# Performance work log

Measured on AMD Instinct MI355X. Metric: run time of the kernel, lower is better.

## Reference

```python
import jax, jax.numpy as jnp
import numpy as np

N, E, G = 8000, 128000, 4
C, NLM, NL = 64, 16, 4
NEL, NB, NH = 10, 8, 64
RMAX = 5.0
PCUT = 5.0
AVG_NEIGH = 16.0
SIGMA = 1.0
LBOX = 6.0
KR = 3
T = 2
LMAP = jnp.array([0, 1, 1, 1, 2, 2, 2, 2, 2, 3, 3, 3, 3, 3, 3, 3])


def _nvec():
    r = np.arange(-KR, KR + 1)
    n = np.stack(np.meshgrid(r, r, r, indexing='ij'), -1).reshape(-1, 3)
    n = n[np.any(n != 0, axis=1)]  # [342,3], k=0 excluded
    return jnp.asarray(n, jnp.float32)


def sph_harm(u):
    # component-normalized real spherical harmonics up to l=3, unit input u [E,3]
    x, y, z = u[:, 0], u[:, 1], u[:, 2]
    one = jnp.ones_like(x)
    c3, c5, c15 = 3.0 ** 0.5, 5.0 ** 0.5, 15.0 ** 0.5
    Y = [one,
         c3 * x, c3 * y, c3 * z,
         c15 * x * y, c15 * y * z, 0.5 * c5 * (3 * z * z - 1.0), c15 * x * z, 0.5 * c15 * (x * x - y * y),
         (35.0 / 8.0) ** 0.5 * y * (3 * x * x - y * y), 105.0 ** 0.5 * x * y * z,
         (21.0 / 8.0) ** 0.5 * y * (5 * z * z - 1.0), 0.5 * 7.0 ** 0.5 * z * (5 * z * z - 3.0),
         (21.0 / 8.0) ** 0.5 * x * (5 * z * z - 1.0), 0.5 * 105.0 ** 0.5 * z * (x * x - y * y),
         (35.0 / 8.0) ** 0.5 * x * (x * x - 3 * y * y)]
    return jnp.stack(Y, -1)  # [E,16]


def radial_basis(r):
    # Bessel basis * polynomial cutoff (MACE RadialEmbeddingBlock)
    u = r / RMAX
    n = jnp.arange(1, NB + 1, dtype=jnp.float32)
    bes = (2.0 / RMAX) ** 0.5 * jnp.sin(n[None, :] * jnp.pi * u[:, None]) / (r[:, None] + 1e-9)
    p = PCUT
    fc = 1.0 - 0.5 * (p + 1) * (p + 2) * u ** p + p * (p + 2) * u ** (p + 1) - 0.5 * p * (p + 1) * u ** (p + 2)
    fc = fc * (u < 1.0)
    return bes * fc[:, None]  # [E,8]


def setup_inputs() -> dict:
    key = jax.random.key(0)
    ks = jax.random.split(key, 24)

    def p(k, shape, fan_in):
        return jax.random.normal(k, shape, jnp.float32) / (fan_in ** 0.5)

    elem = jax.random.randint(ks[0], (N,), 0, NEL)
    inp = {
        'node_attrs': jax.nn.one_hot(elem, NEL, dtype=jnp.float32),
        'positions': jax.random.uniform(ks[1], (N, 3), jnp.float32) * LBOX,
        'shifts': jnp.zeros((E, 3), jnp.float32),
        'density_coefficients': jax.random.normal(ks[2], (N, 1), jnp.float32) * 0.1,
        'cell': jnp.tile(jnp.eye(3, dtype=jnp.float32) * LBOX, (G, 1, 1)),
        'rcell': jnp.tile(jnp.eye(3, dtype=jnp.float32) / LBOX, (G, 1, 1)),
        'volume': jnp.full((G,), LBOX ** 3, jnp.float32),
        'edge_index': jax.random.randint(ks[3], (2, E), 0, N),
        'batch': jnp.repeat(jnp.arange(G), N // G),
        'emb_W': p(ks[4], (NEL, C), NEL),
        'q_coef': p(ks[5], (T, C), 1),
        'rad_W1': p(ks[6], (T, NB, NH), NB),
        'rad_W2': p(ks[7], (T, NH, NH), NH),
        'rad_W3': p(ks[8], (T, NH, NH), NH),
        'rad_W4': p(ks[9], (T, NH, C * NL), NH),
        'lin_up': p(ks[10], (T, NL, C, C), C),
        'lin_out': p(ks[11], (T, NL, C, C), C),
        'W_sc': p(ks[12], (T, NEL, C, C), C),
        'Wp': p(ks[13], (T, 3, C, C), C),
        'W_read0': p(ks[14], (C,), C),
        'Wread1_a': p(ks[15], (C, 16), C),
        'Wread1_b': p(ks[16], (16,), 16),
        'Wq_read': p(ks[17], (T, C), C),
        'atomic_E': jax.random.normal(ks[18], (NEL,), jnp.float32),
    }
    return inp


def reference(node_attrs, positions, shifts, density_coefficients, cell, rcell, volume,
              edge_index, batch, emb_W, q_coef, rad_W1, rad_W2, rad_W3, rad_W4,
              lin_up, lin_out, W_sc, Wp, W_read0, Wread1_a, Wread1_b, Wq_read, atomic_E):
    sender, receiver = edge_index[0], edge_index[1]
    vec = positions[receiver] - positions[sender] + shifts
    r = jnp.linalg.norm(vec, axis=-1)
    Y = sph_harm(vec / (r[:, None] + 1e-9))      # [E,16]
    ef = radial_basis(r)                          # [E,8]

    q = density_coefficients                      # [N,1], max_l=0 multipoles
    feats = jnp.zeros((N, C, NLM), jnp.float32).at[:, :, 0].set(node_attrs @ emb_W)
    e0 = jax.ops.segment_sum(node_attrs @ atomic_E, batch, G)
    energies = [e0]

    for t in range(T):
        # charge-coefficient injection (charge_coefs_linears)
        feats = feats.at[:, :, 0].add(q * q_coef[t][None, :])
        # per-l linear up
        h = jnp.einsum('ncl,lcd->ndl', feats, lin_up[t][LMAP])
        # radial MLP -> per-edge, per-channel, per-l tensor-product weights
        w = jax.nn.silu(ef @ rad_W1[t])
        w = jax.nn.silu(w @ rad_W2[t])
        w = jax.nn.silu(w @ rad_W3[t])
        w = (w @ rad_W4[t]).reshape(E, C, NL)[:, :, LMAP]   # [E,C,16]
        # depthwise equivariant TP message: gather -> contract -> modulate
        hj = h[sender]                                       # [E,C,16]
        s_e = jnp.einsum('ecl,el->ec', hj, Y)                # edge invariant
        m = w * (Y[:, None, :] * s_e[:, :, None])            # [E,C,16]
        A = jax.ops.segment_sum(m, receiver, N) / AVG_NEIGH  # scatter-reduce
        A = jnp.einsum('ncl,lcd->ndl', A, lin_out[t][LMAP])
        # element-dependent residual (self-connection)
        wn = jnp.einsum('nk,kcd->ncd', node_attrs, W_sc[t])
        sc = jnp.einsum('ncd,ncl->ndl', wn, feats)
        # product block: correlation-3 symmetric-contraction surrogate
        s1 = jnp.sum(A * A, axis=2)                           # [N,C]
        out = (jnp.einsum('ncl,cd->ndl', A, Wp[t, 0])
               + jnp.einsum('ncl,cd->ndl', A * s1[:, :, None], Wp[t, 1])
               + jnp.einsum('ncl,cd->ndl', A * (s1 * s1)[:, :, None], Wp[t, 2]))
        feats = out + sc
        # readout
        if t == T - 1:
            node_e = jax.nn.silu(feats[:, :, 0] @ Wread1_a) @ Wread1_b
        else:
            node_e = feats[:, :, 0] @ W_read0
        node_e = node_e + q[:, 0] * (feats[:, :, 0] @ Wq_read[t])
        energies.append(jax.ops.segment_sum(node_e, batch, G))

    # k-space (Ewald-like) electrostatics with Gaussian-smeared charges
    nv = _nvec()                                              # [K,3]
    kvec = 2.0 * jnp.pi * jnp.einsum('kj,gji->gki', nv, rcell)  # [G,K,3]
    k2 = jnp.sum(kvec * kvec, -1)                             # [G,K]
    phase = jnp.einsum('ni,nki->nk', positions, kvec[batch])  # [N,K]
    Sr = jax.ops.segment_sum(q * jnp.cos(phase), batch, G)
    Si = jax.ops.segment_sum(q * jnp.sin(phase), batch, G)
    filt = jnp.exp(-0.5 * SIGMA * SIGMA * k2) / k2
    Ees = (2.0 * jnp.pi / volume) * jnp.sum(filt * (Sr * Sr + Si * Si), axis=1)

    total_energy = jnp.sum(jnp.stack(energies, -1), -1) + Ees
    total_charge = jax.ops.segment_sum(q[:, 0], batch, G)
    dipole = jax.ops.segment_sum(q * positions, batch, G)
    return total_energy, total_charge, dipole
```

## Files before the change

kernel.cpp:

```cpp
#include <hip/hip_runtime.h>
#include <hip/hip_bf16.h>

constexpr int N    = 8000;
constexpr int E    = 128000;
constexpr int G    = 4;
constexpr int NEL  = 10;
constexpr int NGR  = N / G;
constexpr int NC   = N * 64;
constexpr int NK   = 342;
constexpr float RMAX = 5.0f;
constexpr int HS = 72;
constexpr int WS2 = 260;
constexpr int WT_T = 25088;

typedef __bf16 bf16x8 __attribute__((ext_vector_type(8)));
typedef float  f32x4v __attribute__((ext_vector_type(4)));
typedef unsigned short u16x8 __attribute__((ext_vector_type(8)));

__device__ __forceinline__ int lmap_rt(int l) { return (l >= 1) + (l >= 4) + (l >= 9); }
__device__ __forceinline__ float silu(float x) { return x / (1.f + __expf(-x)); }
__device__ __forceinline__ float bf2f(unsigned short u) { return __uint_as_float(((unsigned)u) << 16); }
__device__ __forceinline__ unsigned short f2bf(float f) {
    __hip_bfloat16 h = __float2bfloat16(f);
    return *(unsigned short*)&h;
}

__device__ __forceinline__ void mfma_stage(const unsigned short* hsrc, const unsigned short* wt,
                                           int m0, int lane, f32x4v acc[4], bool k8only)
{
    const int quad = lane >> 4;
    const int idx  = lane & 15;
    bf16x8 bz;
    #pragma unroll
    for (int i = 0; i < 8; ++i) bz[i] = (__bf16)0.f;
    bf16x8 a0 = bz, a1 = bz;
    const int mrow = m0 + idx;
    if (k8only) {
        if (quad == 0) a0 = *(const bf16x8*)&hsrc[mrow * HS];
    } else {
        a0 = *(const bf16x8*)&hsrc[mrow * HS + (quad << 3)];
        a1 = *(const bf16x8*)&hsrc[mrow * HS + 32 + (quad << 3)];
    }
    #pragma unroll
    for (int c4 = 0; c4 < 4; ++c4) {
        const int nrow = (c4 << 4) + idx;
        if (k8only) {
            bf16x8 b0 = bz;
            if (quad == 0) b0 = *(const bf16x8*)&wt[nrow * HS];
            acc[c4] = __builtin_amdgcn_mfma_f32_16x16x32_bf16(a0, b0, acc[c4], 0, 0, 0);
        } else {
            const bf16x8 b0 = *(const bf16x8*)&wt[nrow * HS + (quad << 3)];
            const bf16x8 b1 = *(const bf16x8*)&wt[nrow * HS + 32 + (quad << 3)];
            acc[c4] = __builtin_amdgcn_mfma_f32_16x16x32_bf16(a0, b0, acc[c4], 0, 0, 0);
            acc[c4] = __builtin_amdgcn_mfma_f32_16x16x32_bf16(a1, b1, acc[c4], 0, 0, 0);
        }
    }
}

__global__ __launch_bounds__(256) void k_init(const float* __restrict__ na,
    const float* __restrict__ q, const float* __restrict__ pos,
    const int* __restrict__ batch, const float* __restrict__ aE,
    int* __restrict__ elem, int* __restrict__ counts, float* __restrict__ acc)
{
    __shared__ float s[G * 5];
    if (threadIdx.x < G * 5) s[threadIdx.x] = 0.f;
    __syncthreads();
    const int n = blockIdx.x * 256 + threadIdx.x;
    if (n < N) {
        int el = 0; float best = na[n * NEL];
        #pragma unroll
        for (int j = 1; j < NEL; ++j) { float v = na[n * NEL + j]; if (v > best) { best = v; el = j; } }
        elem[n] = el;
        atomicAdd(&counts[el], 1);
        const int g = batch[n];
        const float qn = q[n];
        atomicAdd(&s[g * 5 + 0], aE[el]);
        atomicAdd(&s[g * 5 + 1], qn);
        atomicAdd(&s[g * 5 + 2], qn * pos[n * 3 + 0]);
        atomicAdd(&s[g * 5 + 3], qn * pos[n * 3 + 1]);
        atomicAdd(&s[g * 5 + 4], qn * pos[n * 3 + 2]);
    }
    __syncthreads();
    if (threadIdx.x < G * 5) atomicAdd(&acc[threadIdx.x], s[threadIdx.x]);
}

__global__ __launch_bounds__(256) void k_feat0(const int* __restrict__ elem,
    const float* __restrict__ embW, unsigned short* __restrict__ Fb)
{
    const int i = blockIdx.x * 256 + threadIdx.x;
    if (i < NC) Fb[i] = f2bf(embW[elem[i >> 6] * 64 + (i & 63)]);
}

__global__ void k_offs(const int* __restrict__ counts, int* __restrict__ offs)
{
    if (threadIdx.x == 0 && blockIdx.x == 0) {
        int o = 0;
        for (int j = 0; j < NEL; ++j) { offs[j] = o; o += (counts[j] + 63) & ~63; }
        offs[NEL] = o;
    }
}
__global__ __launch_bounds__(256) void k_scatter(const int* __restrict__ elem,
    const int* __restrict__ offs, int* __restrict__ cursor, int* __restrict__ perm)
{
    const int n = blockIdx.x * 256 + threadIdx.x;
    if (n < N) {
        const int el = elem[n];
        const int p = atomicAdd(&cursor[el], 1);
        perm[offs[el] + p] = n;
    }
}

__global__ __launch_bounds__(256) void k_gcnt(const int* __restrict__ ei, int* __restrict__ cnt)
{
    const int e = blockIdx.x * 256 + threadIdx.x;
    if (e < E) atomicAdd(&cnt[ei[E + e]], 1);
}
__global__ __launch_bounds__(1024) void k_goff(const int* __restrict__ cnt, int* __restrict__ roff)
{
    __shared__ int part[1024];
    const int t = threadIdx.x;
    const int base = t * 8;
    int loc[8];
    int s = 0;
    #pragma unroll
    for (int i = 0; i < 8; ++i) { loc[i] = s; s += (base + i < N) ? cnt[base + i] : 0; }
    part[t] = s;
    __syncthreads();
    for (int d = 1; d < 1024; d <<= 1) {
        const int v = (t >= d) ? part[t - d] : 0;
        __syncthreads();
        part[t] += v;
        __syncthreads();
    }
    const int excl = (t == 0) ? 0 : part[t - 1];
    #pragma unroll
    for (int i = 0; i < 8; ++i) if (base + i < N) roff[base + i] = excl + loc[i];
    if (t == 0) roff[N] = E;
}
__global__ __launch_bounds__(256) void k_gscat(const int* __restrict__ ei,
    const int* __restrict__ roff, int* __restrict__ cur, int* __restrict__ elist)
{
    const int e = blockIdx.x * 256 + threadIdx.x;
    if (e < E) {
        const int rv = ei[E + e];
        const int p = atomicAdd(&cur[rv], 1);
        elist[roff[rv] + p] = e;
    }
}

__global__ __launch_bounds__(256) void k_geom(const float* __restrict__ pos,
    const float* __restrict__ shifts, const int* __restrict__ ei,
    const int* __restrict__ elist, float4* __restrict__ geomv, int* __restrict__ spck)
{
    const int j = blockIdx.x * 256 + threadIdx.x;
    if (j >= E) return;
    const int e = elist[j];
    const int s = ei[e], rv = ei[E + e];
    const float dx = pos[rv * 3 + 0] - pos[s * 3 + 0] + shifts[e * 3 + 0];
    const float dy = pos[rv * 3 + 1] - pos[s * 3 + 1] + shifts[e * 3 + 1];
    const float dz = pos[rv * 3 + 2] - pos[s * 3 + 2] + shifts[e * 3 + 2];
    const float r = sqrtf(dx * dx + dy * dy + dz * dz);
    const float inv = 1.f / (r + 1e-9f);
    float4 g;
    g.x = dx * inv; g.y = dy * inv; g.z = dz * inv; g.w = r;
    geomv[j] = g;
    spck[j] = s;
}

__global__ __launch_bounds__(256) void k_wprep_all(const float* __restrict__ rW1,
    const float* __restrict__ rW2, const float* __restrict__ rW3,
    const float* __restrict__ rW4, const float* __restrict__ Wp,
    const float* __restrict__ lup, const float* __restrict__ lout,
    const float* __restrict__ Wsc,
    unsigned short* __restrict__ WT, unsigned short* __restrict__ WpT,
    unsigned short* __restrict__ WlupT, unsigned short* __restrict__ WloutT,
    unsigned short* __restrict__ WscT)
{
    const int gidx = blockIdx.x * 256 + threadIdx.x;
    if (gidx < 2 * WT_T) {
        const int t = gidx / WT_T;
        const int r = gidx % WT_T;
        float v;
        if (r < 512) {
            const int n = r >> 3, k = r & 7;
            v = rW1[t * 512 + k * 64 + n];
        } else if (r < 4608) {
            const int i = r - 512, n = i >> 6, k = i & 63;
            v = rW2[t * 4096 + k * 64 + n];
        } else if (r < 8704) {
            const int i = r - 4608, n = i >> 6, k = i & 63;
            v = rW3[t * 4096 + k * 64 + n];
        } else {
            const int i = r - 8704, n = i >> 6, k = i & 63;
            v = rW4[t * 16384 + k * 256 + n];
        }
        WT[gidx] = f2bf(v);
    } else if (gidx < 2 * WT_T + 24576) {
        const int idx = gidx - 2 * WT_T;
        const int i  = idx & 4095;
        const int d = i >> 6, c = i & 63;
        WpT[idx] = f2bf(Wp[(size_t)(idx >> 12) * 4096 + c * 64 + d]);
    } else if (gidx < 2 * WT_T + 24576 + 32768) {
        const int idx = gidx - (2 * WT_T + 24576);
        const int i = idx & 4095, d = i >> 6, c = i & 63;
        WlupT[idx] = f2bf(lup[(idx >> 12) * 4096 + c * 64 + d]);
    } else if (gidx < 2 * WT_T + 24576 + 65536) {
        const int idx = gidx - (2 * WT_T + 24576 + 32768);
        const int i = idx & 4095, d = i >> 6, c = i & 63;
        WloutT[idx] = f2bf(lout[(idx >> 12) * 4096 + c * 64 + d]);
    } else if (gidx < 2 * WT_T + 24576 + 65536 + 81920) {
        const int idx = gidx - (2 * WT_T + 24576 + 65536);
        const int i = idx & 4095, d = i >> 6, c = i & 63;
        WscT[idx] = f2bf(Wsc[(idx >> 12) * 4096 + c * 64 + d]);
    }
}

__global__ __launch_bounds__(256) void k_lgemm_hb(unsigned short* __restrict__ Fb,
    const float* __restrict__ q, const float* __restrict__ qc,
    const unsigned short* __restrict__ WT, unsigned short* __restrict__ Hb)
{
    __shared__ unsigned short Xb[64 * HS];
    __shared__ unsigned short Wt[64 * HS];
    const int l  = blockIdx.y;
    const int nb = blockIdx.x << 6;
    const int t  = threadIdx.x;
    const int lane = t & 63;
    const int m0   = (t >> 6) << 4;
    const int quad = lane >> 4;
    const int idx  = lane & 15;
    const int prow = t >> 2, pkb = (t & 3) << 4;
    unsigned short* Xp = Fb + (size_t)l * NC + (size_t)nb * 64;
    if (l == 0) {
        const float qn = q[nb + prow];
        u16x8 x0 = *(const u16x8*)&Xp[prow * 64 + pkb];
        u16x8 x1 = *(const u16x8*)&Xp[prow * 64 + pkb + 8];
        #pragma unroll
        for (int j = 0; j < 8; ++j) {
            x0[j] = f2bf(bf2f(x0[j]) + qn * qc[pkb + j]);
            x1[j] = f2bf(bf2f(x1[j]) + qn * qc[pkb + 8 + j]);
        }
        *(u16x8*)&Xp[prow * 64 + pkb]     = x0;
        *(u16x8*)&Xp[prow * 64 + pkb + 8] = x1;
        *(u16x8*)&Xb[prow * HS + pkb]     = x0;
        *(u16x8*)&Xb[prow * HS + pkb + 8] = x1;
    } else {
        *(u16x8*)&Xb[prow * HS + pkb]     = *(const u16x8*)&Xp[prow * 64 + pkb];
        *(u16x8*)&Xb[prow * HS + pkb + 8] = *(const u16x8*)&Xp[prow * 64 + pkb + 8];
    }
    const unsigned short* W = WT + lmap_rt(l) * 4096;
    *(u16x8*)&Wt[prow * HS + pkb]     = *(const u16x8*)&W[prow * 64 + pkb];
    *(u16x8*)&Wt[prow * HS + pkb + 8] = *(const u16x8*)&W[prow * 64 + pkb + 8];
    __syncthreads();
    f32x4v acc[4];
    #pragma unroll
    for (int c = 0; c < 4; ++c) { acc[c][0] = 0.f; acc[c][1] = 0.f; acc[c][2] = 0.f; acc[c][3] = 0.f; }
    mfma_stage(Xb, Wt, m0, lane, acc, false);
    #pragma unroll
    for (int c4 = 0; c4 < 4; ++c4) {
        #pragma unroll
        for (int r = 0; r < 4; ++r) {
            const int n = nb + m0 + (quad << 2) + r;
            const int col = (c4 << 4) + idx;
            Hb[(size_t)n * 1024 + (l << 6) + col] = f2bf(acc[c4][r]);
        }
    }
}

__global__ __launch_bounds__(256) void k_hbT(const unsigned short* __restrict__ Hb,
    unsigned short* __restrict__ HbT)
{
    const int n = (blockIdx.x << 2) + (threadIdx.x >> 6);
    const int c = threadIdx.x & 63;
    u16x8 a, b;
    #pragma unroll
    for (int l = 0; l < 8; ++l) {
        a[l] = Hb[(size_t)n * 1024 + (l << 6) + c];
        b[l] = Hb[(size_t)n * 1024 + ((l + 8) << 6) + c];
    }
    *(u16x8*)&HbT[(size_t)n * 1024 + c * 16]     = a;
    *(u16x8*)&HbT[(size_t)n * 1024 + c * 16 + 8] = b;
}

__global__ __launch_bounds__(256) void k_lgemm(const float* __restrict__ X,
    const unsigned short* __restrict__ WT, unsigned short* __restrict__ H2b)
{
    __shared__ unsigned short Xb[64 * HS];
    __shared__ unsigned short Wt[64 * HS];
    const int l  = blockIdx.y;
    const int nb = blockIdx.x << 6;
    const int t  = threadIdx.x;
    const int lane = t & 63;
    const int m0   = (t >> 6) << 4;
    const int quad = lane >> 4;
    const int idx  = lane & 15;
    const int prow = t >> 2, pkb = (t & 3) << 4;
    const float* Xp = X + (size_t)l * NC + (size_t)nb * 64;
    #pragma unroll
    for (int k = 0; k < 16; ++k) {
        const int i = t + (k << 8);
        Xb[(i >> 6) * HS + (i & 63)] = f2bf(Xp[i]);
    }
    const unsigned short* W = WT + lmap_rt(l) * 4096;
    *(u16x8*)&Wt[prow * HS + pkb]     = *(const u16x8*)&W[prow * 64 + pkb];
    *(u16x8*)&Wt[prow * HS + pkb + 8] = *(const u16x8*)&W[prow * 64 + pkb + 8];
    __syncthreads();
    f32x4v acc[4];
    #pragma unroll
    for (int c = 0; c < 4; ++c) { acc[c][0] = 0.f; acc[c][1] = 0.f; acc[c][2] = 0.f; acc[c][3] = 0.f; }
    mfma_stage(Xb, Wt, m0, lane, acc, false);
    unsigned short* Op = H2b + (size_t)l * NC + (size_t)nb * 64;
    #pragma unroll
    for (int c4 = 0; c4 < 4; ++c4) {
        #pragma unroll
        for (int r = 0; r < 4; ++r) {
            const int row = m0 + (quad << 2) + r;
            Op[(row << 6) + (c4 << 4) + idx] = f2bf(acc[c4][r]);
        }
    }
}

__global__ __launch_bounds__(256) void k_sc(const unsigned short* __restrict__ Fb,
    const unsigned short* __restrict__ WscT, const int* __restrict__ perm,
    const int* __restrict__ elem, unsigned short* __restrict__ scb)
{
    __shared__ unsigned short Xb[64 * HS];
    __shared__ unsigned short Wt[64 * HS];
    __shared__ int rows[64];
    const int l  = blockIdx.y;
    const int tb = blockIdx.x << 6;
    const int t  = threadIdx.x;
    if (t < 64) rows[t] = perm[tb + t];
    __syncthreads();
    if (rows[0] < 0) return;
    const int lane = t & 63;
    const int m0   = (t >> 6) << 4;
    const int quad = lane >> 4;
    const int idx  = lane & 15;
    const int prow = t >> 2, pkb = (t & 3) << 4;
    const unsigned short* W = WscT + elem[rows[0]] * 4096;
    *(u16x8*)&Wt[prow * HS + pkb]     = *(const u16x8*)&W[prow * 64 + pkb];
    *(u16x8*)&Wt[prow * HS + pkb + 8] = *(const u16x8*)&W[prow * 64 + pkb + 8];
    {
        const int n = rows[prow];
        u16x8 z;
        #pragma unroll
        for (int j = 0; j < 8; ++j) z[j] = 0;
        u16x8 x0 = z, x1 = z;
        if (n >= 0) {
            const unsigned short* src = Fb + (size_t)l * NC + (size_t)n * 64 + pkb;
            x0 = *(const u16x8*)&src[0];
            x1 = *(const u16x8*)&src[8];
        }
        *(u16x8*)&Xb[prow * HS + pkb]     = x0;
        *(u16x8*)&Xb[prow * HS + pkb + 8] = x1;
    }
    __syncthreads();
    f32x4v acc[4];
    #pragma unroll
    for (int c = 0; c < 4; ++c) { acc[c][0] = 0.f; acc[c][1] = 0.f; acc[c][2] = 0.f; acc[c][3] = 0.f; }
    mfma_stage(Xb, Wt, m0, lane, acc, false);
    #pragma unroll
    for (int c4 = 0; c4 < 4; ++c4) {
        #pragma unroll
        for (int r = 0; r < 4; ++r) {
            const int n = rows[m0 + (quad << 2) + r];
            if (n >= 0) scb[(size_t)l * NC + (size_t)n * 64 + (c4 << 4) + idx] = f2bf(acc[c4][r]);
        }
    }
}

__global__ __launch_bounds__(256) void k_edge(const float4* __restrict__ geomv,
    const int* __restrict__ spck, const unsigned short* __restrict__ WT,
    const unsigned short* __restrict__ HbT, const int* __restrict__ roff,
    float* __restrict__ A)
{
    __shared__ unsigned short hbf[64 * HS];
    __shared__ unsigned short wtb[64 * HS];
    __shared__ unsigned short wfull[64 * WS2];
    __shared__ float geos[64 * 4];
    __shared__ int   sps[64];
    __shared__ int   rinfo[2];
    const int t = threadIdx.x;
    const int lane = t & 63;
    const int wid  = t >> 6;
    const int m0   = wid << 4;
    const int quad = lane >> 4;
    const int idx  = lane & 15;
    const int prow = t >> 2, pkb = (t & 3) << 4;
    const int w0 = blockIdx.x << 6;
    const int w1 = w0 + 64;
    if (t == 0) {
        int lo = 0, hi = N - 1;
        while (lo < hi) { const int mid = (lo + hi + 1) >> 1; if (roff[mid] <= w0) lo = mid; else hi = mid - 1; }
        rinfo[0] = lo;
    } else if (t == 1) {
        const int w1m = w0 + 63;
        int lo = 0, hi = N - 1;
        while (lo < hi) { const int mid = (lo + hi + 1) >> 1; if (roff[mid] <= w1m) lo = mid; else hi = mid - 1; }
        rinfo[1] = lo;
    }
    if (t < 64) {
        const float4 g = geomv[w0 + t];
        *(float4*)&geos[t * 4] = g;
        sps[t] = spck[w0 + t];
        const float r = g.w;
        const float u  = r * 0.2f;
        const float u2 = u * u, u5 = u2 * u2 * u;
        const float fc = 1.f - 21.f * u5 + 35.f * u5 * u - 15.f * u5 * u2;
        float pref = 0.63245553f * fc / (r + 1e-9f);
        if (u >= 1.f) pref = 0.f;
        const float piu = 3.14159265358979f * u;
        #pragma unroll
        for (int b = 0; b < 8; ++b) hbf[t * HS + b] = f2bf(__sinf((float)(b + 1) * piu) * pref);
    }
    {
        const int n = t >> 2, k = (t & 3) << 1;
        wtb[n * HS + k]     = WT[n * 8 + k];
        wtb[n * HS + k + 1] = WT[n * 8 + k + 1];
    }
    u16x8 pf0 = *(const u16x8*)&WT[512 + prow * 64 + pkb];
    u16x8 pf1 = *(const u16x8*)&WT[512 + prow * 64 + pkb + 8];
    __syncthreads();
    f32x4v acc[4];
    #pragma unroll
    for (int c = 0; c < 4; ++c) { acc[c][0] = 0.f; acc[c][1] = 0.f; acc[c][2] = 0.f; acc[c][3] = 0.f; }
    mfma_stage(hbf, wtb, m0, lane, acc, true);
    __syncthreads();
    #pragma unroll
    for (int c4 = 0; c4 < 4; ++c4)
        #pragma unroll
        for (int r = 0; r < 4; ++r)
            hbf[(m0 + (quad << 2) + r) * HS + (c4 << 4) + idx] = f2bf(silu(acc[c4][r]));
    *(u16x8*)&wtb[prow * HS + pkb]     = pf0;
    *(u16x8*)&wtb[prow * HS + pkb + 8] = pf1;
    pf0 = *(const u16x8*)&WT[4608 + prow * 64 + pkb];
    pf1 = *(const u16x8*)&WT[4608 + prow * 64 + pkb + 8];
    __syncthreads();
    #pragma unroll
    for (int c = 0; c < 4; ++c) { acc[c][0] = 0.f; acc[c][1] = 0.f; acc[c][2] = 0.f; acc[c][3] = 0.f; }
    mfma_stage(hbf, wtb, m0, lane, acc, false);
    __syncthreads();
    #pragma unroll
    for (int c4 = 0; c4 < 4; ++c4)
        #pragma unroll
        for (int r = 0; r < 4; ++r)
            hbf[(m0 + (quad << 2) + r) * HS + (c4 << 4) + idx] = f2bf(silu(acc[c4][r]));
    *(u16x8*)&wtb[prow * HS + pkb]     = pf0;
    *(u16x8*)&wtb[prow * HS + pkb + 8] = pf1;
    pf0 = *(const u16x8*)&WT[8704 + prow * 64 + pkb];
    pf1 = *(const u16x8*)&WT[8704 + prow * 64 + pkb + 8];
    __syncthreads();
    #pragma unroll
    for (int c = 0; c < 4; ++c) { acc[c][0] = 0.f; acc[c][1] = 0.f; acc[c][2] = 0.f; acc[c][3] = 0.f; }
    mfma_stage(hbf, wtb, m0, lane, acc, false);
    __syncthreads();
    #pragma unroll
    for (int c4 = 0; c4 < 4; ++c4)
        #pragma unroll
        for (int r = 0; r < 4; ++r)
            hbf[(m0 + (quad << 2) + r) * HS + (c4 << 4) + idx] = f2bf(silu(acc[c4][r]));
    *(u16x8*)&wtb[prow * HS + pkb]     = pf0;
    *(u16x8*)&wtb[prow * HS + pkb + 8] = pf1;
    pf0 = *(const u16x8*)&WT[8704 + 4096 + prow * 64 + pkb];
    pf1 = *(const u16x8*)&WT[8704 + 4096 + prow * 64 + pkb + 8];
    __syncthreads();
    for (int cc = 0; cc < 4; ++cc) {
        #pragma unroll
        for (int c = 0; c < 4; ++c) { acc[c][0] = 0.f; acc[c][1] = 0.f; acc[c][2] = 0.f; acc[c][3] = 0.f; }
        mfma_stage(hbf, wtb, m0, lane, acc, false);
        __syncthreads();
        #pragma unroll
        for (int c4 = 0; c4 < 4; ++c4)
            #pragma unroll
            for (int r = 0; r < 4; ++r)
                wfull[(m0 + (quad << 2) + r) * WS2 + (cc << 6) + (c4 << 4) + idx] = f2bf(acc[c4][r]);
        if (cc < 3) {
            *(u16x8*)&wtb[prow * HS + pkb]     = pf0;
            *(u16x8*)&wtb[prow * HS + pkb + 8] = pf1;
            if (cc < 2) {
                pf0 = *(const u16x8*)&WT[8704 + (cc + 2) * 4096 + prow * 64 + pkb];
                pf1 = *(const u16x8*)&WT[8704 + (cc + 2) * 4096 + prow * 64 + pkb + 8];
            }
        }
        __syncthreads();
    }
    const int r0 = rinfo[0], r1 = rinfo[1];
    constexpr int LM[16] = {0,1,1,1,2,2,2,2,2,3,3,3,3,3,3,3};
    for (int r = r0 + wid; r <= r1; r += 4) {
        const int ra = roff[r], rb = roff[r + 1];
        const int ja = ra > w0 ? ra : w0;
        const int jb = rb < w1 ? rb : w1;
        float a16[16];
        #pragma unroll
        for (int l = 0; l < 16; ++l) a16[l] = 0.f;
        if (ja < jb) {
            u16x8 hA0, hB0, hA1, hB1;
            {
                const int s = sps[ja - w0];
                hA0 = *(const u16x8*)&HbT[(size_t)s * 1024 + lane * 16];
                hB0 = *(const u16x8*)&HbT[(size_t)s * 1024 + lane * 16 + 8];
            }
            hA1 = hA0; hB1 = hB0;
            if (ja + 1 < jb) {
                const int s = sps[ja + 1 - w0];
                hA1 = *(const u16x8*)&HbT[(size_t)s * 1024 + lane * 16];
                hB1 = *(const u16x8*)&HbT[(size_t)s * 1024 + lane * 16 + 8];
            }
            for (int j = ja; j < jb; ++j) {
                const int jj = j - w0;
                float hc[16];
                #pragma unroll
                for (int l = 0; l < 8; ++l) { hc[l] = bf2f(hA0[l]); hc[l + 8] = bf2f(hB0[l]); }
                hA0 = hA1; hB0 = hB1;
                if (j + 2 < jb) {
                    const int s = sps[jj + 2];
                    hA1 = *(const u16x8*)&HbT[(size_t)s * 1024 + lane * 16];
                    hB1 = *(const u16x8*)&HbT[(size_t)s * 1024 + lane * 16 + 8];
                }
                const float gr = geos[jj * 4 + 3];
                if (gr >= RMAX) continue;
                const float x = geos[jj * 4], y = geos[jj * 4 + 1], z = geos[jj * 4 + 2];
                const float xx = x * x, yy = y * y, zz = z * z;
                float Y[16];
                Y[0] = 1.f;
                Y[1] = 1.7320508f * x;  Y[2] = 1.7320508f * y;  Y[3] = 1.7320508f * z;
                Y[4] = 3.8729833f * x * y;  Y[5] = 3.8729833f * y * z;
                Y[6] = 0.5f * 2.2360680f * (3.f * zz - 1.f);
                Y[7] = 3.8729833f * x * z;  Y[8] = 0.5f * 3.8729833f * (xx - yy);
                Y[9]  = 2.0916500f * y * (3.f * xx - yy);
                Y[10] = 10.2469508f * x * y * z;
                Y[11] = 1.6201852f * y * (5.f * zz - 1.f);
                Y[12] = 0.5f * 2.6457513f * z * (5.f * zz - 3.f);
                Y[13] = 1.6201852f * x * (5.f * zz - 1.f);
                Y[14] = 0.5f * 10.2469508f * z * (xx - yy);
                Y[15] = 2.0916500f * x * (xx - 3.f * yy);
                float se = 0.f;
                #pragma unroll
                for (int l = 0; l < 16; ++l) se += hc[l] * Y[l];
                se *= 0.0625f;
                const ushort4 wq = *(const ushort4*)&wfull[jj * WS2 + (lane << 2)];
                const float wl[4] = { bf2f(wq.x) * se, bf2f(wq.y) * se, bf2f(wq.z) * se, bf2f(wq.w) * se };
                #pragma unroll
                for (int l = 0; l < 16; ++l) a16[l] += wl[LM[l]] * Y[l];
            }
        }
        float* Ap = A + (size_t)r * 64 + lane;
        if (ra >= w0 && rb <= w1) {
            #pragma unroll
            for (int l = 0; l < 16; ++l) Ap[(size_t)l * NC] = a16[l];
        } else {
            #pragma unroll
            for (int l = 0; l < 16; ++l) atomicAdd(&Ap[(size_t)l * NC], a16[l]);
        }
    }
}

__global__ __launch_bounds__(256) void k_s1(const unsigned short* __restrict__ H2b, float* __restrict__ s1)
{
    const int i = blockIdx.x * 256 + threadIdx.x;
    if (i < NC) {
        float s = 0.f;
        #pragma unroll
        for (int l = 0; l < 16; ++l) { const float a = bf2f(H2b[(size_t)l * NC + i]); s += a * a; }
        s1[i] = s;
    }
}

__global__ __launch_bounds__(256) void k_out(const unsigned short* __restrict__ H2b,
    const float* __restrict__ s1, const unsigned short* __restrict__ WpT,
    const unsigned short* __restrict__ scb, unsigned short* __restrict__ Fb)
{
    __shared__ unsigned short Xb[64 * HS];
    __shared__ unsigned short Wt[64 * HS];
    const int l  = blockIdx.y;
    const int nb = blockIdx.x << 6;
    const int t  = threadIdx.x;
    const int lane = t & 63;
    const int m0   = (t >> 6) << 4;
    const int quad = lane >> 4;
    const int idx  = lane & 15;
    const int prow = t >> 2, pkb = (t & 3) << 4;
    const unsigned short* Xp = H2b + (size_t)l * NC + (size_t)nb * 64;
    float av[16], sv[16];
    {
        const u16x8 x0 = *(const u16x8*)&Xp[prow * 64 + pkb];
        const u16x8 x1 = *(const u16x8*)&Xp[prow * 64 + pkb + 8];
        #pragma unroll
        for (int j = 0; j < 8; ++j) { av[j] = bf2f(x0[j]); av[8 + j] = bf2f(x1[j]); }
        #pragma unroll
        for (int j = 0; j < 4; ++j) {
            const float4 s4 = *(const float4*)&s1[(nb + prow) * 64 + pkb + (j << 2)];
            sv[j * 4] = s4.x; sv[j * 4 + 1] = s4.y; sv[j * 4 + 2] = s4.z; sv[j * 4 + 3] = s4.w;
        }
    }
    f32x4v acc[4];
    #pragma unroll
    for (int c = 0; c < 4; ++c) { acc[c][0] = 0.f; acc[c][1] = 0.f; acc[c][2] = 0.f; acc[c][3] = 0.f; }
    for (int p = 0; p < 3; ++p) {
        u16x8 x0, x1;
        #pragma unroll
        for (int j = 0; j < 8; ++j) { x0[j] = f2bf(av[j]); x1[j] = f2bf(av[8 + j]); }
        *(u16x8*)&Xb[prow * HS + pkb]     = x0;
        *(u16x8*)&Xb[prow * HS + pkb + 8] = x1;
        #pragma unroll
        for (int k = 0; k < 16; ++k) av[k] *= sv[k];
        *(u16x8*)&Wt[prow * HS + pkb]     = *(const u16x8*)&WpT[p * 4096 + prow * 64 + pkb];
        *(u16x8*)&Wt[prow * HS + pkb + 8] = *(const u16x8*)&WpT[p * 4096 + prow * 64 + pkb + 8];
        __syncthreads();
        mfma_stage(Xb, Wt, m0, lane, acc, false);
        __syncthreads();
    }
    #pragma unroll
    for (int c4 = 0; c4 < 4; ++c4) {
        #pragma unroll
        for (int r = 0; r < 4; ++r) {
            const int row = m0 + (quad << 2) + r;
            const int col = (c4 << 4) + idx;
            const size_t id = (size_t)l * NC + (size_t)(nb + row) * 64 + col;
            Fb[id] = f2bf(acc[c4][r] + bf2f(scb[id]));
        }
    }
}

__global__ __launch_bounds__(256) void k_read(const unsigned short* __restrict__ Fb,
    const float* __restrict__ q, const int* __restrict__ batch,
    const float* __restrict__ Wr0, const float* __restrict__ Wa,
    const float* __restrict__ Wb, const float* __restrict__ Wq,
    float* __restrict__ acc, int last)
{
    __shared__ float sred[G];
    if (threadIdx.x < G) sred[threadIdx.x] = 0.f;
    __syncthreads();
    const int n = blockIdx.x * 256 + threadIdx.x;
    if (n < N) {
        float a16[16];
        #pragma unroll
        for (int j = 0; j < 16; ++j) a16[j] = 0.f;
        float ar = 0.f, aq = 0.f;
        const unsigned short* f = Fb + (size_t)n * 64;
        for (int c = 0; c < 64; ++c) {
            const float fv = bf2f(f[c]);
            aq += fv * Wq[c];
            if (last) {
                #pragma unroll
                for (int j = 0; j < 16; ++j) a16[j] += fv * Wa[c * 16 + j];
            } else ar += fv * Wr0[c];
        }
        float en;
        if (last) {
            en = 0.f;
            #pragma unroll
            for (int j = 0; j < 16; ++j) en += silu(a16[j]) * Wb[j];
        } else en = ar;
        en += q[n] * aq;
        atomicAdd(&sred[batch[n]], en);
    }
    __syncthreads();
    if (threadIdx.x < G) atomicAdd(&acc[threadIdx.x * 5], sred[threadIdx.x]);
}

__global__ __launch_bounds__(256) void k_kvec(const float* __restrict__ rcell,
    float* __restrict__ kvec, float* __restrict__ k2)
{
    const int idx = blockIdx.x * 256 + threadIdx.x;
    if (idx >= G * NK) return;
    const int g = idx / NK, k = idx % NK;
    const int kk = k + (k >= 171 ? 1 : 0);
    const int a = kk / 49 - 3, b = (kk / 7) % 7 - 3, c = kk % 7 - 3;
    const float* rc = rcell + g * 9;
    float s = 0.f;
    #pragma unroll
    for (int i = 0; i < 3; ++i) {
        const float kv = 6.283185307f * ((float)a * rc[0 + i] + (float)b * rc[3 + i] + (float)c * rc[6 + i]);
        kvec[idx * 3 + i] = kv;
        s += kv * kv;
    }
    k2[idx] = s;
}

__global__ __launch_bounds__(256) void k_phase(const float* __restrict__ pos,
    const float* __restrict__ q, const float* __restrict__ kvec,
    float* __restrict__ Sr, float* __restrict__ Si)
{
    __shared__ float kvs[38 * 3];
    __shared__ float srs[38], sis[38];
    const int g = blockIdx.z, kc = blockIdx.x, ncb = blockIdx.y;
    const int kbase = kc * 38;
    if (threadIdx.x < 38 * 3) kvs[threadIdx.x] = kvec[((size_t)g * NK + kbase) * 3 + threadIdx.x];
    if (threadIdx.x < 38) { srs[threadIdx.x] = 0.f; sis[threadIdx.x] = 0.f; }
    __syncthreads();
    const int t = threadIdx.x;
    float px = 0.f, py = 0.f, pz = 0.f, qn = 0.f;
    if (t < 250) {
        const int n = g * NGR + ncb * 250 + t;
        px = pos[n * 3]; py = pos[n * 3 + 1]; pz = pos[n * 3 + 2]; qn = q[n];
    }
    const int lane = t & 63;
    for (int j = 0; j < 38; ++j) {
        const float ph = px * kvs[j * 3] + py * kvs[j * 3 + 1] + pz * kvs[j * 3 + 2];
        float sv, cv;
        __sincosf(ph, &sv, &cv);
        float vr = qn * cv, vi = qn * sv;
        #pragma unroll
        for (int o = 32; o > 0; o >>= 1) { vr += __shfl_down(vr, o, 64); vi += __shfl_down(vi, o, 64); }
        if (lane == 0) { atomicAdd(&srs[j], vr); atomicAdd(&sis[j], vi); }
    }
    __syncthreads();
    if (t < 38) {
        atomicAdd(&Sr[g * NK + kbase + t], srs[t]);
        atomicAdd(&Si[g * NK + kbase + t], sis[t]);
    }
}

__global__ __launch_bounds__(512) void k_final(const float* __restrict__ k2,
    const float* __restrict__ Sr, const float* __restrict__ Si,
    const float* __restrict__ vol, const float* __restrict__ acc,
    float* __restrict__ out)
{
    __shared__ float red[512];
    const int g = blockIdx.x, t = threadIdx.x;
    float v = 0.f;
    if (t < NK) {
        const float kk = k2[g * NK + t];
        const float sr = Sr[g * NK + t], si = Si[g * NK + t];
        v = __expf(-0.5f * kk) * (sr * sr + si * si) / kk;
    }
    red[t] = v;
    __syncthreads();
    for (int s2 = 256; s2 > 0; s2 >>= 1) {
        if (t < s2) red[t] += red[t + s2];
        __syncthreads();
    }
    if (t == 0) {
        const float Ees = 6.283185307f / vol[g] * red[0];
        out[g]     = acc[g * 5 + 0] + Ees;
        out[4 + g] = acc[g * 5 + 1];
        out[8 + g * 3 + 0] = acc[g * 5 + 2];
        out[8 + g * 3 + 1] = acc[g * 5 + 3];
        out[8 + g * 3 + 2] = acc[g * 5 + 4];
    }
}

extern "C" void kernel_launch(void* const* d_in, const int* in_sizes, int n_in,
                              void* d_out, int out_size, void* d_ws, size_t ws_size,
                              hipStream_t stream)
{
    const float* na    = (const float*)d_in[0];
    const float* pos   = (const float*)d_in[1];
    const float* shif  = (const float*)d_in[2];
    const float* q     = (const float*)d_in[3];
    const float* rcell = (const float*)d_in[5];
    const float* vol   = (const float*)d_in[6];
    const int*   ei    = (const int*)d_in[7];
    const int*   batch = (const int*)d_in[8];
    const float* embW  = (const float*)d_in[9];
    const float* qcoef = (const float*)d_in[10];
    const float* rW1   = (const float*)d_in[11];
    const float* rW2   = (const float*)d_in[12];
    const float* rW3   = (const float*)d_in[13];
    const float* rW4   = (const float*)d_in[14];
    const float* lup   = (const float*)d_in[15];
    const float* lout  = (const float*)d_in[16];
    const float* Wsc   = (const float*)d_in[17];
    const float* Wp    = (const float*)d_in[18];
    const float* Wr0   = (const float*)d_in[19];
    const float* Wa    = (const float*)d_in[20];
    const float* Wb    = (const float*)d_in[21];
    const float* Wq    = (const float*)d_in[22];
    const float* aE    = (const float*)d_in[23];
    float* out = (float*)d_out;

    float* wsf  = (float*)d_ws;
    unsigned short* Fb = (unsigned short*)wsf;
    float* A    = wsf + 8192000;
    unsigned short* scb = (unsigned short*)A;
    float* R    = A + 8192000;
    unsigned short* H2b   = (unsigned short*)R;
    unsigned short* HbT   = (unsigned short*)R;
    unsigned short* Hbtmp = (unsigned short*)(R + 4096000);
    float* s1   = R + 20480000;
    float* kvec = s1 + 512000;
    float* k2   = kvec + 4104;
    float* Sr   = k2 + 1368;
    float* Si   = Sr + 1368;
    float* acc  = Si + 1368;
    int*   elem = (int*)(acc + 32);
    int*   perm = elem + 8000;
    int*   counts = perm + 8640;
    int*   cursor = counts + 16;
    int*   offs   = cursor + 16;
    int*   roff   = offs + 16;
    int*   cnt    = roff + 8001;
    int*   cur    = cnt + 8000;
    int*   elist  = cur + 8000;
    unsigned short* WTb = (unsigned short*)(((uintptr_t)(elist + E) + 31) & ~(uintptr_t)31);
    unsigned short* WpT = WTb + 2 * WT_T;
    float4* geomv = (float4*)(WpT + 24576);
    int*    spck  = (int*)(geomv + E);
    unsigned short* WlupT  = (unsigned short*)(spck + E);
    unsigned short* WloutT = WlupT + 32768;
    unsigned short* WscT   = WloutT + 32768;

    hipMemsetAsync(Fb, 0, 8192000 * sizeof(unsigned short), stream);
    hipMemsetAsync(Sr, 0, (1368 * 2 + 32) * sizeof(float), stream);
    hipMemsetAsync(perm, 0xFF, 8640 * sizeof(int), stream);
    hipMemsetAsync(counts, 0, 32 * sizeof(int), stream);
    hipMemsetAsync(cnt, 0, 16000 * sizeof(int), stream);

    k_init<<<32, 256, 0, stream>>>(na, q, pos, batch, aE, elem, counts, acc);
    k_feat0<<<2000, 256, 0, stream>>>(elem, embW, Fb);
    k_offs<<<1, 64, 0, stream>>>(counts, offs);
    k_scatter<<<32, 256, 0, stream>>>(elem, offs, cursor, perm);
    k_gcnt<<<500, 256, 0, stream>>>(ei, cnt);
    k_goff<<<1, 1024, 0, stream>>>(cnt, roff);
    k_gscat<<<500, 256, 0, stream>>>(ei, roff, cur, elist);
    k_geom<<<500, 256, 0, stream>>>(pos, shif, ei, elist, geomv, spck);
    k_wprep_all<<<868, 256, 0, stream>>>(rW1, rW2, rW3, rW4, Wp, lup, lout, Wsc,
                                         WTb, WpT, WlupT, WloutT, WscT);
    k_kvec<<<6, 256, 0, stream>>>(rcell, kvec, k2);
    k_phase<<<dim3(9, 8, G), 256, 0, stream>>>(pos, q, kvec, Sr, Si);

    for (int t = 0; t < 2; ++t) {
        k_lgemm_hb<<<dim3(125, 16), 256, 0, stream>>>(Fb, q, qcoef + t * 64, WlupT + t * 16384, Hbtmp);
        k_hbT<<<2000, 256, 0, stream>>>(Hbtmp, HbT);
        hipMemsetAsync(A, 0, 8192000 * sizeof(float), stream);
        k_edge<<<2000, 256, 0, stream>>>(geomv, spck, WTb + t * WT_T, HbT, roff, A);
        k_lgemm<<<dim3(125, 16), 256, 0, stream>>>(A, WloutT + t * 16384, H2b);
        k_s1<<<2000, 256, 0, stream>>>(H2b, s1);
        k_sc<<<dim3(135, 16), 256, 0, stream>>>(Fb, WscT + t * 40960, perm, elem, scb);
        k_out<<<dim3(125, 16), 256, 0, stream>>>(H2b, s1, WpT + t * 12288, scb, Fb);
        k_read<<<32, 256, 0, stream>>>(Fb, q, batch, Wr0, Wa, Wb, Wq + t * 64, acc, t == 1);
    }
    k_final<<<G, 512, 0, stream>>>(k2, Sr, Si, vol, acc, out);
}
```

Baseline: 533.2 us.

## Precompute edge spherical harmonics per lane and fuse s1 reduction into output kernel

In the edge kernel, each lane now computes the 16 spherical harmonics for its own edge once, with the cutoff applied as a mask. The inner loop fetches them with readlane instead of recomputing Y for every destination row, and the shared geometry buffer is removed. Separately, the k_s1 kernel is folded into a new k_out2, where each block recomputes the squared-norm sum over all 16 l components and then processes 4 l slices, loading all three weight tiles once. This removes a kernel launch and the s1 round trip through memory. The cost is redundant H2b reads, fewer blocks (125x4), and more register pressure in the edge kernel.

```diff
diff --git a/kernel.cpp b/kernel.cpp
--- a/kernel.cpp
+++ b/kernel.cpp
@@ -23,6 +23,9 @@
 __device__ __forceinline__ unsigned short f2bf(float f) {
     __hip_bfloat16 h = __float2bfloat16(f);
     return *(unsigned short*)&h;
+}
+__device__ __forceinline__ float rdlane(float v, int lane) {
+    return __uint_as_float(__builtin_amdgcn_readlane(__float_as_uint(v), lane));
 }
 
 __device__ __forceinline__ void mfma_stage(const unsigned short* hsrc, const unsigned short* wt,
@@ -377,7 +380,6 @@
     __shared__ unsigned short hbf[64 * HS];
     __shared__ unsigned short wtb[64 * HS];
     __shared__ unsigned short wfull[64 * WS2];
-    __shared__ float geos[64 * 4];
     __shared__ int   sps[64];
     __shared__ int   rinfo[2];
     const int t = threadIdx.x;
@@ -399,19 +401,38 @@
         while (lo < hi) { const int mid = (lo + hi + 1) >> 1; if (roff[mid] <= w1m) lo = mid; else hi = mid - 1; }
         rinfo[1] = lo;
     }
-    if (t < 64) {
-        const float4 g = geomv[w0 + t];
-        *(float4*)&geos[t * 4] = g;
-        sps[t] = spck[w0 + t];
-        const float r = g.w;
-        const float u  = r * 0.2f;
-        const float u2 = u * u, u5 = u2 * u2 * u;
-        const float fc = 1.f - 21.f * u5 + 35.f * u5 * u - 15.f * u5 * u2;
-        float pref = 0.63245553f * fc / (r + 1e-9f);
-        if (u >= 1.f) pref = 0.f;
-        const float piu = 3.14159265358979f * u;
-        #pragma unroll
-        for (int b = 0; b < 8; ++b) hbf[t * HS + b] = f2bf(__sinf((float)(b + 1) * piu) * pref);
+    float yreg[16];
+    {
+        const float4 g = geomv[w0 + lane];
+        const float x = g.x, y = g.y, z = g.z;
+        const float xx = x * x, yy = y * y, zz = z * z;
+        yreg[0] = 1.f;
+        yreg[1] = 1.7320508f * x;  yreg[2] = 1.7320508f * y;  yreg[3] = 1.7320508f * z;
+        yreg[4] = 3.8729833f * x * y;  yreg[5] = 3.8729833f * y * z;
+        yreg[6] = 0.5f * 2.2360680f * (3.f * zz - 1.f);
+        yreg[7] = 3.8729833f * x * z;  yreg[8] = 0.5f * 3.8729833f * (xx - yy);
+        yreg[9]  = 2.0916500f * y * (3.f * xx - yy);
+        yreg[10] = 10.2469508f * x * y * z;
+        yreg[11] = 1.6201852f * y * (5.f * zz - 1.f);
+        yreg[12] = 0.5f * 2.6457513f * z * (5.f * zz - 3.f);
+        yreg[13] = 1.6201852f * x * (5.f * zz - 1.f);
+        yreg[14] = 0.5f * 10.2469508f * z * (xx - yy);
+        yreg[15] = 2.0916500f * x * (xx - 3.f * yy);
+        const float m = (g.w < RMAX) ? 1.f : 0.f;
+        #pragma unroll
+        for (int l = 0; l < 16; ++l) yreg[l] *= m;
+        if (t < 64) {
+            sps[t] = spck[w0 + t];
+            const float r = g.w;
+            const float u  = r * 0.2f;
+            const float u2 = u * u, u5 = u2 * u2 * u;
+            const float fc = 1.f - 21.f * u5 + 35.f * u5 * u - 15.f * u5 * u2;
+            float pref = 0.63245553f * fc / (r + 1e-9f);
+            if (u >= 1.f) pref = 0.f;
+            const float piu = 3.14159265358979f * u;
+            #pragma unroll
+            for (int b = 0; b < 8; ++b) hbf[t * HS + b] = f2bf(__sinf((float)(b + 1) * piu) * pref);
+        }
     }
     {
         const int n = t >> 2, k = (t & 3) << 1;
@@ -517,31 +538,17 @@
                     hA1 = *(const u16x8*)&HbT[(size_t)s * 1024 + lane * 16];
                     hB1 = *(const u16x8*)&HbT[(size_t)s * 1024 + lane * 16 + 8];
                 }
-                const float gr = geos[jj * 4 + 3];
-                if (gr >= RMAX) continue;
-                const float x = geos[jj * 4], y = geos[jj * 4 + 1], z = geos[jj * 4 + 2];
-                const float xx = x * x, yy = y * y, zz = z * z;
-                float Y[16];
-                Y[0] = 1.f;
-                Y[1] = 1.7320508f * x;  Y[2] = 1.7320508f * y;  Y[3] = 1.7320508f * z;
-                Y[4] = 3.8729833f * x * y;  Y[5] = 3.8729833f * y * z;
-                Y[6] = 0.5f * 2.2360680f * (3.f * zz - 1.f);
-                Y[7] = 3.8729833f * x * z;  Y[8] = 0.5f * 3.8729833f * (xx - yy);
-                Y[9]  = 2.0916500f * y * (3.f * xx - yy);
-                Y[10] = 10.2469508f * x * y * z;
-                Y[11] = 1.6201852f * y * (5.f * zz - 1.f);
-                Y[12] = 0.5f * 2.6457513f * z * (5.f * zz - 3.f);
-                Y[13] = 1.6201852f * x * (5.f * zz - 1.f);
-                Y[14] = 0.5f * 10.2469508f * z * (xx - yy);
-                Y[15] = 2.0916500f * x * (xx - 3.f * yy);
+                float sY[16];
+                #pragma unroll
+                for (int l = 0; l < 16; ++l) sY[l] = rdlane(yreg[l], jj);
                 float se = 0.f;
                 #pragma unroll
-                for (int l = 0; l < 16; ++l) se += hc[l] * Y[l];
+                for (int l = 0; l < 16; ++l) se += hc[l] * sY[l];
                 se *= 0.0625f;
                 const ushort4 wq = *(const ushort4*)&wfull[jj * WS2 + (lane << 2)];
                 const float wl[4] = { bf2f(wq.x) * se, bf2f(wq.y) * se, bf2f(wq.z) * se, bf2f(wq.w) * se };
                 #pragma unroll
-                for (int l = 0; l < 16; ++l) a16[l] += wl[LM[l]] * Y[l];
+                for (int l = 0; l < 16; ++l) a16[l] += wl[LM[l]] * sY[l];
             }
         }
         float* Ap = A + (size_t)r * 64 + lane;
@@ -555,69 +562,73 @@
     }
 }
 
-__global__ __launch_bounds__(256) void k_s1(const unsigned short* __restrict__ H2b, float* __restrict__ s1)
-{
-    const int i = blockIdx.x * 256 + threadIdx.x;
-    if (i < NC) {
-        float s = 0.f;
-        #pragma unroll
-        for (int l = 0; l < 16; ++l) { const float a = bf2f(H2b[(size_t)l * NC + i]); s += a * a; }
-        s1[i] = s;
-    }
-}
-
-__global__ __launch_bounds__(256) void k_out(const unsigned short* __restrict__ H2b,
-    const float* __restrict__ s1, const unsigned short* __restrict__ WpT,
-    const unsigned short* __restrict__ scb, unsigned short* __restrict__ Fb)
+__global__ __launch_bounds__(256) void k_out2(const unsigned short* __restrict__ H2b,
+    const unsigned short* __restrict__ WpT, const unsigned short* __restrict__ scb,
+    unsigned short* __restrict__ Fb)
 {
     __shared__ unsigned short Xb[64 * HS];
-    __shared__ unsigned short Wt[64 * HS];
-    const int l  = blockIdx.y;
+    __shared__ unsigned short Wt3[3][64 * HS];
     const int nb = blockIdx.x << 6;
+    const int lq = blockIdx.y;
     const int t  = threadIdx.x;
     const int lane = t & 63;
     const int m0   = (t >> 6) << 4;
     const int quad = lane >> 4;
     const int idx  = lane & 15;
     const int prow = t >> 2, pkb = (t & 3) << 4;
-    const unsigned short* Xp = H2b + (size_t)l * NC + (size_t)nb * 64;
-    float av[16], sv[16];
-    {
+    #pragma unroll
+    for (int p = 0; p < 3; ++p) {
+        *(u16x8*)&Wt3[p][prow * HS + pkb]     = *(const u16x8*)&WpT[p * 4096 + prow * 64 + pkb];
+        *(u16x8*)&Wt3[p][prow * HS + pkb + 8] = *(const u16x8*)&WpT[p * 4096 + prow * 64 + pkb + 8];
+    }
+    float sv[16];
+    #pragma unroll
+    for (int k = 0; k < 16; ++k) sv[k] = 0.f;
+    for (int l = 0; l < 16; ++l) {
+        const unsigned short* Xp = H2b + (size_t)l * NC + (size_t)nb * 64;
         const u16x8 x0 = *(const u16x8*)&Xp[prow * 64 + pkb];
         const u16x8 x1 = *(const u16x8*)&Xp[prow * 64 + pkb + 8];
         #pragma unroll
-        for (int j = 0; j < 8; ++j) { av[j] = bf2f(x0[j]); av[8 + j] = bf2f(x1[j]); }
-        #pragma unroll
-        for (int j = 0; j < 4; ++j) {
-            const float4 s4 = *(const float4*)&s1[(nb + prow) * 64 + pkb + (j << 2)];
-            sv[j * 4] = s4.x; sv[j * 4 + 1] = s4.y; sv[j * 4 + 2] = s4.z; sv[j * 4 + 3] = s4.w;
-        }
-    }
-    f32x4v acc[4];
-    #pragma unroll
-    for (int c = 0; c < 4; ++c) { acc[c][0] = 0.f; acc[c][1] = 0.f; acc[c][2] = 0.f; acc[c][3] = 0.f; }
-    for (int p = 0; p < 3; ++p) {
-        u16x8 x0, x1;
-        #pragma unroll
-        for (int j = 0; j < 8; ++j) { x0[j] = f2bf(av[j]); x1[j] = f2bf(av[8 + j]); }
-        *(u16x8*)&Xb[prow * HS + pkb]     = x0;
-        *(u16x8*)&Xb[prow * HS + pkb + 8] = x1;
-        #pragma unroll
-        for (int k = 0; k < 16; ++k) av[k] *= sv[k];
-        *(u16x8*)&Wt[prow * HS + pkb]     = *(const u16x8*)&WpT[p * 4096 + prow * 64 + pkb];
-        *(u16x8*)&Wt[prow * HS + pkb + 8] = *(const u16x8*)&WpT[p * 4096 + prow * 64 + pkb + 8];
-        __syncthreads();
-        mfma_stage(Xb, Wt, m0, lane, acc, false);
-        __syncthreads();
-    }
-    #pragma unroll
-    for (int c4 = 0; c4 < 4; ++c4) {
-        #pragma unroll
-        for (int r = 0; r < 4; ++r) {
-            const int row = m0 + (quad << 2) + r;
-            const int col = (c4 << 4) + idx;
-            const size_t id = (size_t)l * NC + (size_t)(nb + row) * 64 + col;
-            Fb[id] = f2bf(acc[c4][r] + bf2f(scb[id]));
+        for (int j = 0; j < 8; ++j) {
+            const float a = bf2f(x0[j]); sv[j] += a * a;
+            const float b = bf2f(x1[j]); sv[8 + j] += b * b;
+        }
+    }
+    __syncthreads();
+    for (int li = 0; li < 4; ++li) {
+        const int l = (lq << 2) + li;
+        const unsigned short* Xp = H2b + (size_t)l * NC + (size_t)nb * 64;
+        float av[16];
+        {
+            const u16x8 x0 = *(const u16x8*)&Xp[prow * 64 + pkb];
+            const u16x8 x1 = *(const u16x8*)&Xp[prow * 64 + pkb + 8];
+            #pragma unroll
+            for (int j = 0; j < 8; ++j) { av[j] = bf2f(x0[j]); av[8 + j] = bf2f(x1[j]); }
+        }
+        f32x4v acc[4];
+        #pragma unroll
+        for (int c = 0; c < 4; ++c) { acc[c][0] = 0.f; acc[c][1] = 0.f; acc[c][2] = 0.f; acc[c][3] = 0.f; }
+        for (int p = 0; p < 3; ++p) {
+            u16x8 x0, x1;
+            #pragma unroll
+            for (int j = 0; j < 8; ++j) { x0[j] = f2bf(av[j]); x1[j] = f2bf(av[8 + j]); }
+            *(u16x8*)&Xb[prow * HS + pkb]     = x0;
+            *(u16x8*)&Xb[prow * HS + pkb + 8] = x1;
+            #pragma unroll
+            for (int k = 0; k < 16; ++k) av[k] *= sv[k];
+            __syncthreads();
+            mfma_stage(Xb, Wt3[p], m0, lane, acc, false);
+            __syncthreads();
+        }
+        #pragma unroll
+        for (int c4 = 0; c4 < 4; ++c4) {
+            #pragma unroll
+            for (int r = 0; r < 4; ++r) {
+                const int row = m0 + (quad << 2) + r;
+                const int col = (c4 << 4) + idx;
+                const size_t id = (size_t)l * NC + (size_t)(nb + row) * 64 + col;
+                Fb[id] = f2bf(acc[c4][r] + bf2f(scb[id]));
+            }
         }
     }
 }
@@ -826,9 +837,8 @@
         hipMemsetAsync(A, 0, 8192000 * sizeof(float), stream);
         k_edge<<<2000, 256, 0, stream>>>(geomv, spck, WTb + t * WT_T, HbT, roff, A);
         k_lgemm<<<dim3(125, 16), 256, 0, stream>>>(A, WloutT + t * 16384, H2b);
-        k_s1<<<2000, 256, 0, stream>>>(H2b, s1);
         k_sc<<<dim3(135, 16), 256, 0, stream>>>(Fb, WscT + t * 40960, perm, elem, scb);
-        k_out<<<dim3(125, 16), 256, 0, stream>>>(H2b, s1, WpT + t * 12288, scb, Fb);
+        k_out2<<<dim3(125, 4), 256, 0, stream>>>(H2b, WpT + t * 12288, scb, Fb);
         k_read<<<32, 256, 0, stream>>>(Fb, q, batch, Wr0, Wa, Wb, Wq + t * 64, acc, t == 1);
     }
     k_final<<<G, 512, 0, stream>>>(k2, Sr, Si, vol, acc, out);
```

Result: slower. 552.0 us (+3.5%).
